# Optimization experiments

Hardware: AMD Instinct MI355X
Metric: run time of the kernel (lower is better)

Reference implementation:

```python
import jax, jax.numpy as jnp
import numpy as np

DIM, HEADS, WIN, SHIFT = 384, 12, 7, 3
H, W = 56, 56
HEAD_DIM = DIM // HEADS
SCALE = HEAD_DIM ** -0.5
N = WIN * WIN


def _relative_index():
    coords = np.stack(np.meshgrid(np.arange(WIN), np.arange(WIN), indexing='ij')).reshape(2, -1)
    rel = (coords[:, :, None] - coords[:, None, :]).transpose(1, 2, 0)
    rel[:, :, 0] += WIN - 1
    rel[:, :, 1] += WIN - 1
    rel[:, :, 0] *= 2 * WIN - 1
    return rel.sum(-1)  # [N, N] int


def _attn_mask():
    img = np.zeros((H, W), dtype=np.float32)
    cnt = 0
    sls = (slice(0, -WIN), slice(-WIN, -SHIFT), slice(-SHIFT, None))
    for hs in sls:
        for ws in sls:
            img[hs, ws] = cnt
            cnt += 1
    m = img.reshape(H // WIN, WIN, W // WIN, WIN).transpose(0, 2, 1, 3).reshape(-1, N)  # [nw, N]
    diff = m[:, None, :] - m[:, :, None]  # [nw, N, N]
    return np.where(diff != 0, -10000.0, 0.0).astype(np.float32)

REL_IDX = jnp.asarray(_relative_index())
MASK = jnp.asarray(_attn_mask())  # [nw, N, N]


def _layernorm(x, w, b):
    mu = x.mean(-1, keepdims=True)
    var = ((x - mu) ** 2).mean(-1, keepdims=True)
    return (x - mu) * jax.lax.rsqrt(var + 1e-5) * w + b


def _window_partition(x):  # [B,H,W,C] -> [B*nw, N, C]
    B, _, _, C = x.shape
    x = x.reshape(B, H // WIN, WIN, W // WIN, WIN, C)
    x = x.transpose(0, 1, 3, 2, 4, 5)
    return x.reshape(-1, N, C)


def _window_reverse(w, B):  # [B*nw, N, C] -> [B,H,W,C]
    C = w.shape[-1]
    x = w.reshape(B, H // WIN, W // WIN, WIN, WIN, C)
    x = x.transpose(0, 1, 3, 2, 4, 5)
    return x.reshape(B, H, W, C)


def setup_inputs() -> dict:
    key = jax.random.key(0)
    ks = jax.random.split(key, 12)
    s = DIM ** -0.5
    return {
        'x': jax.random.normal(ks[0], (32, H * W, DIM), jnp.float32),
        'qkv_w': jax.random.normal(ks[1], (DIM, 3 * DIM), jnp.float32) * s,  # stored [in,out]
        'qkv_b': jnp.zeros((3 * DIM,), jnp.float32),
        'proj_w': jax.random.normal(ks[2], (DIM, DIM), jnp.float32) * s,
        'proj_b': jnp.zeros((DIM,), jnp.float32),
        'rel_bias': jax.random.normal(ks[3], ((2 * WIN - 1) ** 2, HEADS), jnp.float32) * 0.02,
        'norm1_w': jnp.ones((DIM,), jnp.float32),
        'norm1_b': jnp.zeros((DIM,), jnp.float32),
        'norm2_w': jnp.ones((DIM,), jnp.float32),
        'norm2_b': jnp.zeros((DIM,), jnp.float32),
        'mlp_w1': jax.random.normal(ks[4], (DIM, 4 * DIM), jnp.float32) * s,
        'mlp_b1': jnp.zeros((4 * DIM,), jnp.float32),
        'mlp_w2': jax.random.normal(ks[5], (4 * DIM, DIM), jnp.float32) * (4 * DIM) ** -0.5,
        'mlp_b2': jnp.zeros((DIM,), jnp.float32),
    }


def _forward(x, qkv_w, qkv_b, proj_w, proj_b, rel_bias, norm1_w, norm1_b,
             norm2_w, norm2_b, mlp_w1, mlp_b1, mlp_w2, mlp_b2):
    B, L, C = x.shape
    residual = x
    h = _layernorm(x, norm1_w, norm1_b).reshape(B, H, W, C)
    h = jnp.roll(h, (-SHIFT, -SHIFT), axis=(1, 2))
    wx = _window_partition(h)  # [B_, N, C]
    B_ = wx.shape[0]

    qkv = (wx @ qkv_w + qkv_b).reshape(B_, N, 3, HEADS, HEAD_DIM)
    q, k, v = qkv[:, :, 0], qkv[:, :, 1], qkv[:, :, 2]  # [B_, N, h, d]
    attn = jnp.einsum('bnhd,bmhd->bhnm', q * SCALE, k)  # [B_, h, N, N]
    rb = rel_bias[REL_IDX.reshape(-1)].reshape(N, N, HEADS).transpose(2, 0, 1)
    attn = attn + rb[None]
    nw = MASK.shape[0]
    attn = attn.reshape(B_ // nw, nw, HEADS, N, N) + MASK[None, :, None]
    attn = jax.nn.softmax(attn.reshape(B_, HEADS, N, N), axis=-1)
    out = jnp.einsum('bhnm,bmhd->bnhd', attn, v).reshape(B_, N, C)
    out = out @ proj_w + proj_b

    h = _window_reverse(out, B)
    h = jnp.roll(h, (SHIFT, SHIFT), axis=(1, 2))
    x = h.reshape(B, L, C) + residual

    m = _layernorm(x, norm2_w, norm2_b)
    m = jax.nn.gelu(m @ mlp_w1 + mlp_b1, approximate=False) @ mlp_w2 + mlp_b2
    return x + m


def reference(x, qkv_w, qkv_b, proj_w, proj_b, rel_bias, norm1_w, norm1_b,
              norm2_w, norm2_b, mlp_w1, mlp_b1, mlp_w2, mlp_b2):
    return _forward(x, qkv_w, qkv_b, proj_w, proj_b, rel_bias, norm1_w, norm1_b,
                    norm2_w, norm2_b, mlp_w1, mlp_b1, mlp_w2, mlp_b2)
```

## Files before the change

### kernel.cpp

```cpp
#include <hip/hip_runtime.h>
#include <hip/hip_bf16.h>

typedef unsigned short u16;
typedef __bf16 bf16x8 __attribute__((ext_vector_type(8)));
typedef float f32x4 __attribute__((ext_vector_type(4)));

#define HH 56
#define WW 56
#define DIM 384
#define NTOK 100352
#define NWIN 2048
#define NN 49

__device__ __forceinline__ u16 f2bf(float f) {
    __hip_bfloat16 h = __float2bfloat16(f);
    return *reinterpret_cast<u16*>(&h);
}
__device__ __forceinline__ float bf2f(u16 u) {
    union { unsigned int i; float f; } c; c.i = ((unsigned int)u) << 16; return c.f;
}

__device__ __forceinline__ float fast_gelu(float x) {
    float au = fabsf(x) * 0.70710678118654752f;
    float t = __builtin_amdgcn_rcpf(fmaf(0.3275911f, au, 1.0f));
    float p = fmaf(t, 1.061405429f, -1.453152027f);
    p = fmaf(t, p, 1.421413741f);
    p = fmaf(t, p, -0.284496736f);
    p = fmaf(t, p, 0.254829592f);
    p = p * t;
    float e = __expf(-au * au);
    float erfau = fmaf(-p, e, 1.0f);
    float erfx = __builtin_copysignf(erfau, x);
    return 0.5f * x * (1.0f + erfx);
}

#define GLD_LDS(gp, lp) __builtin_amdgcn_global_load_lds( \
    (const __attribute__((address_space(1))) void*)(gp), \
    (__attribute__((address_space(3))) void*)(lp), 16, 0, 0)

__global__ __launch_bounds__(256) void castT_all(
    const float* __restrict__ qkv_w, const float* __restrict__ proj_w,
    const float* __restrict__ w1, const float* __restrict__ w2,
    u16* __restrict__ qkv_wt, u16* __restrict__ proj_wt,
    u16* __restrict__ w1t, u16* __restrict__ w2t)
{
    int b = blockIdx.x;
    const float* in; u16* out; int K, N, tile;
    if (b < 432)       { in = qkv_w;  out = qkv_wt;  K = 384;  N = 1152; tile = b; }
    else if (b < 576)  { in = proj_w; out = proj_wt; K = 384;  N = 384;  tile = b - 432; }
    else if (b < 1152) { in = w1;     out = w1t;     K = 384;  N = 1536; tile = b - 576; }
    else               { in = w2;     out = w2t;     K = 1536; N = 384;  tile = b - 1152; }
    const int ncols = N >> 5;
    const int tn = tile % ncols, tk = tile / ncols;
    const int n0 = tn * 32, k0 = tk * 32;
    __shared__ float ts[32][33];
    const int tr = threadIdx.x >> 3;
    const int tc = (threadIdx.x & 7) * 4;
    const float4 v = *(const float4*)(in + (size_t)(k0 + tr) * N + n0 + tc);
    ts[tr][tc] = v.x; ts[tr][tc+1] = v.y; ts[tr][tc+2] = v.z; ts[tr][tc+3] = v.w;
    __syncthreads();
    u16 o4[4];
    o4[0] = f2bf(ts[tc][tr]);     o4[1] = f2bf(ts[tc+1][tr]);
    o4[2] = f2bf(ts[tc+2][tr]);   o4[3] = f2bf(ts[tc+3][tr]);
    *(uint2*)(out + (size_t)(n0 + tr) * K + k0 + tc) = *(uint2*)o4;
}

__global__ void bias_kernel(const float* __restrict__ rel_bias, float* __restrict__ Tb) {
    int ty = blockIdx.x / 12, h = blockIdx.x - ty * 12;
    for (int i = threadIdx.x; i < 4096; i += 256) {
        int q = i >> 6, kk = i & 63;
        float v;
        if (kk >= 49) v = -1e30f;
        else if (q >= 49) v = 0.f;
        else {
            int rn = q / 7, cn = q - rn * 7;
            int rm = kk / 7, cm = kk - rm * 7;
            float rb = rel_bias[((rn - rm + 6) * 13 + (cn - cm + 6)) * 12 + h];
            int h0 = (ty >> 1) ? 49 : 0;
            int w0 = (ty & 1) ? 49 : 0;
            int hn = h0 + rn, hm = h0 + rm, wn = w0 + cn, wm = w0 + cm;
            int regn = (hn < 49 ? 0 : (hn < 53 ? 1 : 2)) * 3 + (wn < 49 ? 0 : (wn < 53 ? 1 : 2));
            int regm = (hm < 49 ? 0 : (hm < 53 ? 1 : 2)) * 3 + (wm < 49 ? 0 : (wm < 53 ? 1 : 2));
            v = rb + ((regn == regm) ? 0.f : -10000.f);
        }
        Tb[(size_t)blockIdx.x * 4096 + i] = v;
    }
}

template<bool WIN_MAP>
__global__ __launch_bounds__(256) void ln_kernel(
    const float* __restrict__ x, const float* __restrict__ w, const float* __restrict__ b,
    u16* __restrict__ out)
{
    int token = blockIdx.x * 4 + (threadIdx.x >> 6);
    int lane = threadIdx.x & 63;
    const float* row = x + (size_t)token * DIM;
    float v[6]; float sum = 0.f, sq = 0.f;
#pragma unroll
    for (int j = 0; j < 3; j++) {
        float2 p = *(const float2*)(row + lane * 2 + j * 128);
        v[2*j] = p.x; v[2*j+1] = p.y;
        sum += p.x + p.y; sq += p.x * p.x + p.y * p.y;
    }
#pragma unroll
    for (int off = 32; off; off >>= 1) { sum += __shfl_xor(sum, off); sq += __shfl_xor(sq, off); }
    float mu = sum * (1.f / DIM);
    float rstd = rsqrtf(sq * (1.f / DIM) - mu * mu + 1e-5f);
    size_t obase;
    if (WIN_MAP) {
        int b_ = token / 3136, hw = token - b_ * 3136;
        int h = hw / WW, wc_ = hw - h * WW;
        int hr = h - 3; if (hr < 0) hr += HH;
        int wr = wc_ - 3; if (wr < 0) wr += WW;
        int win = b_ * 64 + (hr / 7) * 8 + (wr / 7);
        int n = (hr % 7) * 7 + (wr % 7);
        obase = ((size_t)win * NN + n) * DIM;
    } else {
        obase = (size_t)token * DIM;
    }
#pragma unroll
    for (int j = 0; j < 3; j++) {
        int c = lane * 2 + j * 128;
        float a0 = (v[2*j]   - mu) * rstd * w[c]   + b[c];
        float a1 = (v[2*j+1] - mu) * rstd * w[c+1] + b[c+1];
        unsigned int pair = (unsigned int)f2bf(a0) | ((unsigned int)f2bf(a1) << 16);
        *(unsigned int*)(out + obase + c) = pair;
    }
}

template<int EPI, bool REV>
__global__ __launch_bounds__(512, 4) void gemm_kernel(
    const u16* __restrict__ A, const u16* __restrict__ Bt,
    const float* __restrict__ bias, const float* __restrict__ resid,
    void* __restrict__ outp, int N, int K, int BNT)
{
    __shared__ u16 sA[2][8192];
    __shared__ u16 sB[2][4096];
    const int tid = threadIdx.x;
    const int lane = tid & 63;
    const int wave = tid >> 6;
    const int wr = wave >> 1, wc = wave & 1;

    const int q8 = gridDim.x >> 3;
    int wg = (blockIdx.x & 7) * q8 + (blockIdx.x >> 3);
    if (REV) wg = gridDim.x - 1 - wg;
    const int bm = wg / BNT, bn = wg - bm * BNT;

    f32x4 acc[4][4] = {};

    const int r0 = tid >> 2;
    const int sg = (tid & 3) ^ (r0 & 3) ^ ((r0 >> 2) & 3);
    const u16* Arow0 = A + (size_t)(bm * 256 + r0) * K + sg * 8;
    const u16* Arow1 = Arow0 + (size_t)128 * K;
    const u16* Brow0 = Bt + (size_t)(bn * 128 + r0) * K + sg * 8;

    const int nt = K >> 5;

#define STAGE(t, buf) do { \
        int kt_ = (t) * 32; \
        GLD_LDS(Arow0 + kt_, &sA[buf][wave * 512]); \
        GLD_LDS(Arow1 + kt_, &sA[buf][4096 + wave * 512]); \
        GLD_LDS(Brow0 + kt_, &sB[buf][wave * 512]); \
    } while (0)

    STAGE(0, 0); STAGE(1, 1);

    const int l15 = lane & 15, g = lane >> 4;
    const int ssr = (g ^ (l15 & 3) ^ ((l15 >> 2) & 3)) * 8;

    for (int t = 0; t < nt; t++) {
        const int bsel = t & 1;
        if (t + 1 < nt) asm volatile("s_waitcnt vmcnt(3)" ::: "memory");
        else            asm volatile("s_waitcnt vmcnt(0)" ::: "memory");
        __builtin_amdgcn_s_barrier();
        __builtin_amdgcn_sched_barrier(0);
        bf16x8 af[4], bfr[4];
#pragma unroll
        for (int m = 0; m < 4; m++) {
            int row = wr * 64 + m * 16 + l15;
            af[m] = *(const bf16x8*)&sA[bsel][row * 32 + ssr];
        }
#pragma unroll
        for (int n = 0; n < 4; n++) {
            int row = wc * 64 + n * 16 + l15;
            bfr[n] = *(const bf16x8*)&sB[bsel][row * 32 + ssr];
        }
        asm volatile("s_waitcnt lgkmcnt(0)" ::: "memory");
        __builtin_amdgcn_sched_barrier(0);
        __builtin_amdgcn_s_barrier();
        __builtin_amdgcn_sched_barrier(0);
        if (t + 2 < nt) STAGE(t + 2, bsel);
#pragma unroll
        for (int m = 0; m < 4; m++)
#pragma unroll
            for (int n = 0; n < 4; n++)
                acc[m][n] = __builtin_amdgcn_mfma_f32_16x16x32_bf16(af[m], bfr[n], acc[m][n], 0, 0, 0);
    }
#undef STAGE

    const int col0 = bn * 128 + wc * 64 + l15;
    float bias4[4];
#pragma unroll
    for (int nn = 0; nn < 4; nn++) bias4[nn] = bias[col0 + nn * 16];

#pragma unroll
    for (int m = 0; m < 4; m++) {
#pragma unroll
        for (int r = 0; r < 4; r++) {
            int row = bm * 256 + wr * 64 + m * 16 + (g << 2) + r;
            size_t obase;
            if (EPI == 1) {
                int win = row / NN, n = row - win * NN;
                int b_ = win >> 6, wi = win & 63;
                int hr = (wi >> 3) * 7 + n / 7;
                int wcl = (wi & 7) * 7 + n % 7;
                int hf = hr + 3; if (hf >= HH) hf -= HH;
                int wf = wcl + 3; if (wf >= WW) wf -= WW;
                obase = ((size_t)b_ * 3136 + hf * WW + wf) * DIM;
            } else {
                obase = (size_t)row * N;
            }
#pragma unroll
            for (int nn = 0; nn < 4; nn++) {
                int col = col0 + nn * 16;
                float val = acc[m][nn][r] + bias4[nn];
                if (EPI == 0) {
                    ((u16*)outp)[obase + col] = f2bf(val);
                } else if (EPI == 1) {
                    ((float*)outp)[obase + col] = val + resid[obase + col];
                } else if (EPI == 2) {
                    ((u16*)outp)[obase + col] = f2bf(fast_gelu(val));
                } else {
                    ((float*)outp)[obase + col] = val + resid[obase + col];
                }
            }
        }
    }
}

__global__ __launch_bounds__(256) void attn_kernel(
    const u16* __restrict__ qkv, const float* __restrict__ Tb,
    u16* __restrict__ attn_out)
{
    __shared__ u16 smem[4][6912];
    const int win = blockIdx.x;
    const int wave = threadIdx.x >> 6;
    const int lane = threadIdx.x & 63;
    const int head = blockIdx.y * 4 + wave;
    const int l15 = lane & 15, g = lane >> 4;

    u16* Vt = smem[wave];
    u16* P  = Vt + 2304;

    const u16* qkvw = qkv + (size_t)win * NN * 1152 + head * 32;

    {
        int m = lane;
        bool real = m < NN;
        const u16* vrow = qkvw + (size_t)(real ? m : 0) * 1152 + 768;
        int4 z = {0,0,0,0};
        int4 c0 = real ? *(const int4*)(vrow)      : z;
        int4 c1 = real ? *(const int4*)(vrow + 8)  : z;
        int4 c2 = real ? *(const int4*)(vrow + 16) : z;
        int4 c3 = real ? *(const int4*)(vrow + 24) : z;
        u16 vals[32];
        *(int4*)&vals[0]  = c0; *(int4*)&vals[8]  = c1;
        *(int4*)&vals[16] = c2; *(int4*)&vals[24] = c3;
#pragma unroll
        for (int d = 0; d < 32; d++) Vt[d * 72 + m] = vals[d];
    }

    bf16x8 kf[4], qf[4];
#pragma unroll
    for (int t = 0; t < 4; t++) {
        int row = t * 16 + l15; if (row > 48) row = 48;
        const u16* base = qkvw + (size_t)row * 1152 + g * 8;
        kf[t] = *(const bf16x8*)(base + 384);
        qf[t] = *(const bf16x8*)(base);
    }
    f32x4 s[4][4];
#pragma unroll
    for (int mt = 0; mt < 4; mt++)
#pragma unroll
        for (int nt = 0; nt < 4; nt++) {
            f32x4 zero = {};
            s[mt][nt] = __builtin_amdgcn_mfma_f32_16x16x32_bf16(kf[mt], qf[nt], zero, 0, 0, 0);
        }

    const int wi = win & 63;
    const int ty = (((wi >> 3) == 7) ? 2 : 0) + (((wi & 7) == 7) ? 1 : 0);
    const float* tbb = Tb + (((size_t)ty * 12 + head) << 12);
    const float SCALE = 0.17677669529663687f;
#pragma unroll
    for (int nt = 0; nt < 4; nt++) {
        int q = nt * 16 + l15;
        const float* trow = tbb + q * 64 + g * 4;
        f32x4 b[4];
#pragma unroll
        for (int mt = 0; mt < 4; mt++) b[mt] = *(const f32x4*)(trow + mt * 16);
        float mx = -3e38f;
#pragma unroll
        for (int mt = 0; mt < 4; mt++)
#pragma unroll
            for (int r = 0; r < 4; r++) {
                float v = s[mt][nt][r] * SCALE + b[mt][r];
                s[mt][nt][r] = v;
                mx = fmaxf(mx, v);
            }
        mx = fmaxf(mx, __shfl_xor(mx, 16));
        mx = fmaxf(mx, __shfl_xor(mx, 32));
        float sum = 0.f;
#pragma unroll
        for (int mt = 0; mt < 4; mt++)
#pragma unroll
            for (int r = 0; r < 4; r++) {
                float e = __expf(s[mt][nt][r] - mx);
                s[mt][nt][r] = e;
                sum += e;
            }
        sum += __shfl_xor(sum, 16);
        sum += __shfl_xor(sum, 32);
        float inv = 1.f / sum;
#pragma unroll
        for (int mt = 0; mt < 4; mt++) {
            unsigned int p01 = (unsigned int)f2bf(s[mt][nt][0] * inv) | ((unsigned int)f2bf(s[mt][nt][1] * inv) << 16);
            unsigned int p23 = (unsigned int)f2bf(s[mt][nt][2] * inv) | ((unsigned int)f2bf(s[mt][nt][3] * inv) << 16);
            uint2 pk; pk.x = p01; pk.y = p23;
            *(uint2*)&P[(unsigned)q * 72 + mt * 16 + g * 4] = pk;
        }
    }

    bf16x8 vf[2][2];
#pragma unroll
    for (int ks = 0; ks < 2; ks++)
#pragma unroll
        for (int dt = 0; dt < 2; dt++)
            vf[ks][dt] = *(const bf16x8*)&Vt[(dt * 16 + l15) * 72 + ks * 32 + g * 8];

    f32x4 o[4][2] = {};
#pragma unroll
    for (int nt = 0; nt < 4; nt++) {
        bf16x8 pf0 = *(const bf16x8*)&P[(nt * 16 + l15) * 72 + g * 8];
        bf16x8 pf1 = *(const bf16x8*)&P[(nt * 16 + l15) * 72 + 32 + g * 8];
#pragma unroll
        for (int dt = 0; dt < 2; dt++) {
            o[nt][dt] = __builtin_amdgcn_mfma_f32_16x16x32_bf16(pf0, vf[0][dt], o[nt][dt], 0, 0, 0);
            o[nt][dt] = __builtin_amdgcn_mfma_f32_16x16x32_bf16(pf1, vf[1][dt], o[nt][dt], 0, 0, 0);
        }
    }

#pragma unroll
    for (int nt = 0; nt < 4; nt++)
#pragma unroll
        for (int r = 0; r < 4; r++) {
            int q = nt * 16 + 4 * g + r;
            if (q < NN) {
                size_t ob = ((size_t)win * NN + q) * DIM + head * 32;
                attn_out[ob + l15]      = f2bf(o[nt][0][r]);
                attn_out[ob + 16 + l15] = f2bf(o[nt][1][r]);
            }
        }
}

extern "C" void kernel_launch(void* const* d_in, const int* in_sizes, int n_in,
                              void* d_out, int out_size, void* d_ws, size_t ws_size,
                              hipStream_t stream)
{
    const float* x      = (const float*)d_in[0];
    const float* qkv_w  = (const float*)d_in[1];
    const float* qkv_b  = (const float*)d_in[2];
    const float* proj_w = (const float*)d_in[3];
    const float* proj_b = (const float*)d_in[4];
    const float* rel_b  = (const float*)d_in[5];
    const float* n1w    = (const float*)d_in[6];
    const float* n1b    = (const float*)d_in[7];
    const float* n2w    = (const float*)d_in[8];
    const float* n2b    = (const float*)d_in[9];
    const float* w1     = (const float*)d_in[10];
    const float* b1     = (const float*)d_in[11];
    const float* w2     = (const float*)d_in[12];
    const float* b2     = (const float*)d_in[13];

    char* ws = (char*)d_ws;
    u16* hidden  = (u16*)(ws);
    u16* qkvbuf  = hidden;
    float* Tb    = (float*)(ws + 231211008);
    u16* wxbuf   = (u16*)(ws + 308281344);
    u16* qkv_wt  = (u16*)(ws + 385351680);
    u16* proj_wt = (u16*)(ws + 386236416);
    u16* w1t     = (u16*)(ws + 386531328);
    u16* w2t     = (u16*)(ws + 387710976);

    castT_all<<<1728, 256, 0, stream>>>(qkv_w, proj_w, w1, w2, qkv_wt, proj_wt, w1t, w2t);
    bias_kernel<<<48, 256, 0, stream>>>(rel_b, Tb);

    ln_kernel<true><<<NTOK / 4, 256, 0, stream>>>(x, n1w, n1b, wxbuf);
    gemm_kernel<0, true><<<392 * 9, 512, 0, stream>>>(wxbuf, qkv_wt, qkv_b, nullptr, qkvbuf, 1152, 384, 9);
    attn_kernel<<<dim3(NWIN, 3), 256, 0, stream>>>(qkvbuf, Tb, wxbuf);
    gemm_kernel<1, true><<<392 * 3, 512, 0, stream>>>(wxbuf, proj_wt, proj_b, x, d_out, 384, 384, 3);
    ln_kernel<false><<<NTOK / 4, 256, 0, stream>>>((const float*)d_out, n2w, n2b, wxbuf);
    gemm_kernel<2, true><<<392 * 12, 512, 0, stream>>>(wxbuf, w1t, b1, nullptr, hidden, 1536, 384, 12);
    gemm_kernel<3, false><<<392 * 3, 512, 0, stream>>>(hidden, w2t, b2, (const float*)d_out, d_out, 384, 1536, 3);
}
```

Before: 863.9 us.

## Add 256x256-tile GEMM kernel for QKV and MLP projections

Adds a new 1024-thread GEMM kernel with 256x256 output tiles, double-buffered LDS staging and swizzled shared-memory reads, and uses it for the QKV, MLP-up and MLP-down GEMMs. Larger tiles raise arithmetic intensity and cut redundant global loads of A and B. Where N is not a multiple of 256 (1152, 384) the padded columns are computed and skipped via NVALID, which wastes MFMA work. The weight buffers are moved so the padded B reads stay inside valid workspace. The 1024-thread blocks may also lower occupancy and add register pressure.

```diff
diff --git a/kernel.cpp b/kernel.cpp
--- a/kernel.cpp
+++ b/kernel.cpp
@@ -238,6 +238,105 @@
     }
 }
 
+template<int EPI, bool REV, int NVALID>
+__global__ __launch_bounds__(1024, 4) void gemm256(
+    const u16* __restrict__ A, const u16* __restrict__ Bt,
+    const float* __restrict__ bias, const float* __restrict__ resid,
+    void* __restrict__ outp, int N, int K, int BNT)
+{
+    __shared__ u16 sA[2][8192];
+    __shared__ u16 sB[2][8192];
+    const int tid = threadIdx.x;
+    const int lane = tid & 63;
+    const int wave = tid >> 6;
+    const int wr = wave >> 2, wc = wave & 3;
+
+    const int q8 = gridDim.x >> 3;
+    int wg = (blockIdx.x & 7) * q8 + (blockIdx.x >> 3);
+    if (REV) wg = gridDim.x - 1 - wg;
+    const int bm = wg / BNT, bn = wg - bm * BNT;
+
+    f32x4 acc[4][4] = {};
+
+    const int r0 = tid >> 2;
+    const int sg = (tid & 3) ^ (r0 & 3) ^ ((r0 >> 2) & 3);
+    const u16* Arow = A + (size_t)(bm * 256 + r0) * K + sg * 8;
+    const u16* Brow = Bt + (size_t)(bn * 256 + r0) * K + sg * 8;
+
+    const int nt = K >> 5;
+
+#define STAGE(t, buf) do { \
+        int kt_ = (t) * 32; \
+        GLD_LDS(Arow + kt_, &sA[buf][wave * 512]); \
+        GLD_LDS(Brow + kt_, &sB[buf][wave * 512]); \
+    } while (0)
+
+    STAGE(0, 0); STAGE(1, 1);
+
+    const int l15 = lane & 15, g = lane >> 4;
+    const int ssr = (g ^ (l15 & 3) ^ ((l15 >> 2) & 3)) * 8;
+
+    for (int t = 0; t < nt; t++) {
+        const int bsel = t & 1;
+        if (t + 1 < nt) asm volatile("s_waitcnt vmcnt(2)" ::: "memory");
+        else            asm volatile("s_waitcnt vmcnt(0)" ::: "memory");
+        __builtin_amdgcn_s_barrier();
+        __builtin_amdgcn_sched_barrier(0);
+        bf16x8 af[4], bfr[4];
+#pragma unroll
+        for (int m = 0; m < 4; m++) {
+            int row = wr * 64 + m * 16 + l15;
+            af[m] = *(const bf16x8*)&sA[bsel][row * 32 + ssr];
+        }
+#pragma unroll
+        for (int n = 0; n < 4; n++) {
+            int row = wc * 64 + n * 16 + l15;
+            bfr[n] = *(const bf16x8*)&sB[bsel][row * 32 + ssr];
+        }
+        asm volatile("s_waitcnt lgkmcnt(0)" ::: "memory");
+        __builtin_amdgcn_sched_barrier(0);
+        __builtin_amdgcn_s_barrier();
+        __builtin_amdgcn_sched_barrier(0);
+        if (t + 2 < nt) STAGE(t + 2, bsel);
+#pragma unroll
+        for (int m = 0; m < 4; m++)
+#pragma unroll
+            for (int n = 0; n < 4; n++)
+                acc[m][n] = __builtin_amdgcn_mfma_f32_16x16x32_bf16(af[m], bfr[n], acc[m][n], 0, 0, 0);
+    }
+#undef STAGE
+
+    const int col0 = bn * 256 + wc * 64 + l15;
+    float bias4[4];
+#pragma unroll
+    for (int nn = 0; nn < 4; nn++) {
+        int col = col0 + nn * 16;
+        bias4[nn] = (NVALID == 0 || col < NVALID) ? bias[col] : 0.f;
+    }
+
+#pragma unroll
+    for (int m = 0; m < 4; m++) {
+#pragma unroll
+        for (int r = 0; r < 4; r++) {
+            int row = bm * 256 + wr * 64 + m * 16 + (g << 2) + r;
+            size_t obase = (size_t)row * N;
+#pragma unroll
+            for (int nn = 0; nn < 4; nn++) {
+                int col = col0 + nn * 16;
+                if (NVALID != 0 && col >= NVALID) continue;
+                float val = acc[m][nn][r] + bias4[nn];
+                if (EPI == 0) {
+                    ((u16*)outp)[obase + col] = f2bf(val);
+                } else if (EPI == 2) {
+                    ((u16*)outp)[obase + col] = f2bf(fast_gelu(val));
+                } else {
+                    ((float*)outp)[obase + col] = val + resid[obase + col];
+                }
+            }
+        }
+    }
+}
+
 __global__ __launch_bounds__(256) void attn_kernel(
     const u16* __restrict__ qkv, const float* __restrict__ Tb,
     u16* __restrict__ attn_out)
@@ -385,20 +484,20 @@
     u16* hidden  = (u16*)(ws);
     u16* qkvbuf  = hidden;
     float* Tb    = (float*)(ws + 231211008);
+    u16* qkv_wt  = (u16*)(ws + 231997440);
     u16* wxbuf   = (u16*)(ws + 308281344);
-    u16* qkv_wt  = (u16*)(ws + 385351680);
-    u16* proj_wt = (u16*)(ws + 386236416);
-    u16* w1t     = (u16*)(ws + 386531328);
-    u16* w2t     = (u16*)(ws + 387710976);
+    u16* proj_wt = (u16*)(ws + 385351680);
+    u16* w1t     = (u16*)(ws + 385646592);
+    u16* w2t     = (u16*)(ws + 386826240);
 
     castT_all<<<1728, 256, 0, stream>>>(qkv_w, proj_w, w1, w2, qkv_wt, proj_wt, w1t, w2t);
     bias_kernel<<<48, 256, 0, stream>>>(rel_b, Tb);
 
     ln_kernel<true><<<NTOK / 4, 256, 0, stream>>>(x, n1w, n1b, wxbuf);
-    gemm_kernel<0, true><<<392 * 9, 512, 0, stream>>>(wxbuf, qkv_wt, qkv_b, nullptr, qkvbuf, 1152, 384, 9);
+    gemm256<0, true, 1152><<<392 * 5, 1024, 0, stream>>>(wxbuf, qkv_wt, qkv_b, nullptr, qkvbuf, 1152, 384, 5);
     attn_kernel<<<dim3(NWIN, 3), 256, 0, stream>>>(qkvbuf, Tb, wxbuf);
     gemm_kernel<1, true><<<392 * 3, 512, 0, stream>>>(wxbuf, proj_wt, proj_b, x, d_out, 384, 384, 3);
     ln_kernel<false><<<NTOK / 4, 256, 0, stream>>>((const float*)d_out, n2w, n2b, wxbuf);
-    gemm_kernel<2, true><<<392 * 12, 512, 0, stream>>>(wxbuf, w1t, b1, nullptr, hidden, 1536, 384, 12);
-    gemm_kernel<3, false><<<392 * 3, 512, 0, stream>>>(hidden, w2t, b2, (const float*)d_out, d_out, 384, 1536, 3);
-}
+    gemm256<2, true, 0><<<392 * 6, 1024, 0, stream>>>(wxbuf, w1t, b1, nullptr, hidden, 1536, 384, 6);
+    gemm256<3, false, 384><<<392 * 2, 1024, 0, stream>>>(hidden, w2t, b2, (const float*)d_out, d_out, 384, 1536, 2);
+}
```

Result: slower. 1.137 ms (+31.6%).
